# Performance work log

Measured on AMD Instinct MI355X. Metric: run time of the kernel, lower is better.

Reference implementation:

```python
import jax, jax.numpy as jnp
import numpy as np

N = 50000          # num nodes
E = 600000         # num edges
F_IN = 128         # num_features
H = 128            # graph_hidden_dim
R = 2              # num_relations
L = 3              # n_layers_conv
BN_EPS = 1e-5
BN_BETA = 1e-4     # BatchNorm bias init per module code


def setup_inputs() -> dict:
    key = jax.random.key(0)
    ks = jax.random.split(key, 9)
    s_in = 1.0 / np.sqrt(F_IN)
    s_h = 1.0 / np.sqrt(H)
    return {
        "x": jax.random.normal(ks[0], (N, F_IN), jnp.float32),
        "edge_index": jax.random.randint(ks[1], (2, E), 0, N, jnp.int32),
        "edge_type": jax.random.randint(ks[2], (E,), 0, R, jnp.int32),
        "W0_rel": jax.random.normal(ks[3], (R, F_IN, H), jnp.float32) * s_in,
        "W0_root": jax.random.normal(ks[4], (F_IN, H), jnp.float32) * s_in,
        "b0": jnp.zeros((H,), jnp.float32),
        "Ws_rel": jax.random.normal(ks[5], (L, R, H, H), jnp.float32) * s_h,
        "Ws_root": jax.random.normal(ks[6], (L, H, H), jnp.float32) * s_h,
        "bs": jnp.zeros((L, H), jnp.float32),
    }


def batchnorm(x):
    # training-mode BatchNorm1d over nodes; weight=1, bias=1e-4 (per init)
    mu = jnp.mean(x, axis=0)
    var = jnp.mean((x - mu) ** 2, axis=0)  # biased var, as torch uses for norm
    return (x - mu) * jax.lax.rsqrt(var + BN_EPS) + BN_BETA


def rgcn_conv(x, src, dst, edge_type, W_rel, W_root, b):
    # PyG RGCNConv, aggr='mean': per-relation mean of x[src] at dst,
    # then per-relation linear, plus root transform and bias.
    seg = dst * R + edge_type  # combined (node, relation) segment id
    msgs = x[src]                                   # [E, d] gather
    sums = jax.ops.segment_sum(msgs, seg, num_segments=N * R)
    cnts = jax.ops.segment_sum(jnp.ones((src.shape[0],), x.dtype), seg,
                               num_segments=N * R)
    mean = sums.reshape(N, R, -1) / jnp.maximum(cnts, 1.0).reshape(N, R, 1)
    out = jnp.einsum('nrd,rdh->nh', mean, W_rel) + x @ W_root + b
    return out


def reference(x, edge_index, edge_type, W0_rel, W0_root, b0, Ws_rel, Ws_root, bs):
    src, dst = edge_index[0], edge_index[1]
    h = batchnorm(x)
    h = jax.nn.relu(rgcn_conv(h, src, dst, edge_type, W0_rel, W0_root, b0))
    for i in range(L):
        h_ = batchnorm(h)
        h_ = jax.nn.relu(rgcn_conv(h_, src, dst, edge_type,
                                   Ws_rel[i], Ws_root[i], bs[i]))
        h = h + h_  # conv_residual=True
    return h  # gconv_dropout == 0
```

## Files before the change

kernel.cpp:

```cpp
#include <hip/hip_runtime.h>
#include <hip/hip_bf16.h>

#define N_NODES 50000
#define N_EDGES 600000
#define F 128
#define R 2
#define NLAYER 4
#define NSEG (N_NODES * R)
#define SEGP (NSEG / 8)
#define NSCB 98
#define NB 384
#define STATS_STRIDE 2048
#define AGGB 6250
#define BN_EPS 1e-5f
#define BETA 1e-4f

typedef __hip_bfloat16 bf16;
typedef __attribute__((ext_vector_type(8))) short short8;
typedef __attribute__((ext_vector_type(4))) short short4x;
typedef __attribute__((ext_vector_type(4))) float floatx4;

__device__ __forceinline__ float b2f(short s) {
    union { unsigned u; float f; } c;
    c.u = ((unsigned)(unsigned short)s) << 16;
    return c.f;
}

__global__ void k_wt(const float* __restrict__ W0_rel, const float* __restrict__ W0_root,
                     const float* __restrict__ Ws_rel, const float* __restrict__ Ws_root,
                     bf16* __restrict__ Bt) {
    int idx = blockIdx.x * 256 + threadIdx.x;
    if (idx >= NLAYER * NB * F) return;
    int l = idx / (NB * F);
    int rem = idx % (NB * F);
    int j = rem / F, d = rem % F;
    float v;
    if (j < 256) {
        int r = j >> 7, c = j & 127;
        v = (l == 0) ? W0_rel[(r * F + d) * F + c]
                     : Ws_rel[((size_t)((l - 1) * R + r) * F + d) * F + c];
    } else {
        int c = j - 256;
        v = (l == 0) ? W0_root[d * F + c]
                     : Ws_root[((size_t)(l - 1) * F + d) * F + c];
    }
    Bt[idx] = __float2bfloat16(v);
}

__global__ void k_seg(const int* __restrict__ dst, const int* __restrict__ et,
                      int* __restrict__ seg) {
    int e = blockIdx.x * 256 + threadIdx.x;
    if (e < N_EDGES) seg[e] = dst[e] * R + et[e];
}

__global__ void k_count(const int* __restrict__ seg, int* __restrict__ cnt) {
    int g = blockIdx.x & 7;
    int lo = g * SEGP, hi = lo + SEGP;
    for (int e = (blockIdx.x >> 3) * 256 + threadIdx.x; e < N_EDGES; e += 65536) {
        int s = seg[e];
        if (s >= lo && s < hi) atomicAdd(&cnt[s], 1);
    }
}

__global__ void k_scan1(const int* __restrict__ cnt, int* __restrict__ off,
                        int* __restrict__ bsum) {
    int t = threadIdx.x;
    int g = blockIdx.x * 1024 + t;
    int v = (g < NSEG) ? cnt[g] : 0;
    int lane = t & 63;
    int wv = t >> 6;
    int x = v;
    for (int d = 1; d < 64; d <<= 1) {
        int y = __shfl_up(x, d, 64);
        if (lane >= d) x += y;
    }
    __shared__ int wtot[16];
    if (lane == 63) wtot[wv] = x;
    __syncthreads();
    if (t < 16) {
        int s = wtot[t];
        for (int d = 1; d < 16; d <<= 1) {
            int y = __shfl_up(s, d, 64);
            if (t >= d) s += y;
        }
        wtot[t] = s;
    }
    __syncthreads();
    int wpre = (wv == 0) ? 0 : wtot[wv - 1];
    int incl = x + wpre;
    if (g < NSEG) off[g] = incl - v;
    if (t == 1023) bsum[blockIdx.x] = incl;
}

__global__ void k_scan3(int* __restrict__ off, const int* __restrict__ bsum) {
    __shared__ int pre;
    if (threadIdx.x == 0) {
        int p = 0;
        for (int b = 0; b < blockIdx.x; b++) p += bsum[b];
        pre = p;
    }
    __syncthreads();
    int g = blockIdx.x * 1024 + threadIdx.x;
    if (g < NSEG) off[g] += pre;
}

__global__ void k_fill(const int* __restrict__ src, const int* __restrict__ seg,
                       const int* __restrict__ off,
                       int* __restrict__ fill, int* __restrict__ esrc) {
    int g = blockIdx.x & 7;
    int lo = g * SEGP, hi = lo + SEGP;
    for (int e = (blockIdx.x >> 3) * 256 + threadIdx.x; e < N_EDGES; e += 65536) {
        int s = seg[e];
        if (s >= lo && s < hi) {
            int idx = off[s] + atomicAdd(&fill[s], 1);
            esrc[idx] = src[e];
        }
    }
}

__global__ void k_bnstats(const float* __restrict__ h, float* __restrict__ gs) {
    int c = threadIdx.x & 127;
    int rl = threadIdx.x >> 7;
    float s = 0.f, q = 0.f;
    for (int r = blockIdx.x * 2 + rl; r < N_NODES; r += gridDim.x * 2) {
        float v = h[(size_t)r * F + c];
        s += v; q += v * v;
    }
    __shared__ float ls[256], lq[256];
    ls[threadIdx.x] = s; lq[threadIdx.x] = q;
    __syncthreads();
    if (rl == 0) {
        atomicAdd(&gs[c], ls[c] + ls[c + 128]);
        atomicAdd(&gs[128 + c], lq[c] + lq[c + 128]);
    }
}

__launch_bounds__(512)
__global__ void k_gemm(const void* __restrict__ hin, int in_bf16,
                       const float* __restrict__ gs,
                       const bf16* __restrict__ Bt, const float* __restrict__ bias,
                       bf16* __restrict__ y, bf16* __restrict__ z) {
    __shared__ bf16 As[64 * 136];
    __shared__ bf16 Bs[128 * 136];
    int t = threadIdx.x;
    int m0 = blockIdx.x * 64;
    int c4 = (t & 31) * 4;
    float mu[4], rs[4];
    for (int c = 0; c < 4; c++) {
        float ssum = 0.f, qsum = 0.f;
        #pragma unroll
        for (int k = 0; k < 8; k++) {
            ssum += gs[k * 256 + c4 + c];
            qsum += gs[k * 256 + 128 + c4 + c];
        }
        float mm = ssum * (1.0f / N_NODES);
        float qq = qsum * (1.0f / N_NODES);
        mu[c] = mm;
        rs[c] = rsqrtf(qq - mm * mm + BN_EPS);
    }
    short8 cur[4], nxt[4];
    #pragma unroll
    for (int rr = 0; rr < 4; rr++) {
        int idx = rr * 512 + t;
        int row = idx >> 4;
        int kc = idx & 15;
        cur[rr] = *(const short8*)(Bt + row * F + kc * 8);
    }
    int r0 = t >> 5;
    for (int it = 0; it < 4; it++) {
        int row = r0 + it * 16;
        int m = m0 + row;
        float f0 = 0.f, f1 = 0.f, f2 = 0.f, f3 = 0.f;
        if (m < N_NODES) {
            if (in_bf16) {
                short4x v = *(const short4x*)((const bf16*)hin + (size_t)m * F + c4);
                f0 = b2f(v.x); f1 = b2f(v.y); f2 = b2f(v.z); f3 = b2f(v.w);
            } else {
                float4 v = *(const float4*)((const float*)hin + (size_t)m * F + c4);
                f0 = v.x; f1 = v.y; f2 = v.z; f3 = v.w;
            }
        }
        bf16 o[4];
        o[0] = __float2bfloat16((f0 - mu[0]) * rs[0] + BETA);
        o[1] = __float2bfloat16((f1 - mu[1]) * rs[1] + BETA);
        o[2] = __float2bfloat16((f2 - mu[2]) * rs[2] + BETA);
        o[3] = __float2bfloat16((f3 - mu[3]) * rs[3] + BETA);
        *(double*)(As + row * 136 + c4) = *(const double*)o;
    }
    __syncthreads();
    int w = t >> 6;
    int lane = t & 63;
    int msub = w & 3;
    int nh = w >> 2;
    int lm = lane & 15;
    int lq = lane >> 4;
    short8 a[4];
    for (int ki = 0; ki < 4; ki++)
        a[ki] = *(const short8*)(As + (msub * 16 + lm) * 136 + ki * 32 + lq * 8);
    int m = m0 + msub * 16 + lm;
    #pragma unroll
    for (int ci = 0; ci < 3; ci++) {
        #pragma unroll
        for (int rr = 0; rr < 4; rr++) {
            int idx = rr * 512 + t;
            int row = idx >> 4;
            int kc = idx & 15;
            *(short8*)(Bs + row * 136 + kc * 8) = cur[rr];
        }
        if (ci < 2) {
            const bf16* bsrc = Bt + (size_t)(ci + 1) * 128 * F;
            #pragma unroll
            for (int rr = 0; rr < 4; rr++) {
                int idx = rr * 512 + t;
                int row = idx >> 4;
                int kc = idx & 15;
                nxt[rr] = *(const short8*)(bsrc + row * F + kc * 8);
            }
        }
        __syncthreads();
        for (int tt = 0; tt < 4; tt++) {
            int nt = nh * 4 + tt;
            short8 b[4];
            for (int ki = 0; ki < 4; ki++)
                b[ki] = *(const short8*)(Bs + (nt * 16 + lm) * 136 + ki * 32 + lq * 8);
            floatx4 acc = {0.f, 0.f, 0.f, 0.f};
            for (int ki = 0; ki < 4; ki++)
                acc = __builtin_amdgcn_mfma_f32_16x16x32_bf16(b[ki], a[ki], acc, 0, 0, 0);
            int n0 = ci * 128 + nt * 16 + lq * 4;
            if (m < N_NODES) {
                if (ci < 2) {
                    union { bf16 o[4]; double d; } u;
                    u.o[0] = __float2bfloat16(acc[0]);
                    u.o[1] = __float2bfloat16(acc[1]);
                    u.o[2] = __float2bfloat16(acc[2]);
                    u.o[3] = __float2bfloat16(acc[3]);
                    *(double*)(y + (size_t)m * 256 + n0) = u.d;
                } else {
                    float4 bv = *(const float4*)(bias + (n0 - 256));
                    union { bf16 o[4]; double d; } u;
                    u.o[0] = __float2bfloat16(acc[0] + bv.x);
                    u.o[1] = __float2bfloat16(acc[1] + bv.y);
                    u.o[2] = __float2bfloat16(acc[2] + bv.z);
                    u.o[3] = __float2bfloat16(acc[3] + bv.w);
                    *(double*)(z + (size_t)m * F + (n0 - 256)) = u.d;
                }
            }
        }
        if (ci < 2) {
            __syncthreads();
            #pragma unroll
            for (int rr = 0; rr < 4; rr++) cur[rr] = nxt[rr];
        }
    }
}

__launch_bounds__(512)
__global__ void k_aggregate(const bf16* __restrict__ y, const bf16* __restrict__ z,
                            const int* __restrict__ cnt, const int* __restrict__ off,
                            const int* __restrict__ esrc,
                            const bf16* __restrict__ hres, bf16* __restrict__ hb_out,
                            float* __restrict__ out_f32,
                            float* __restrict__ gs_next, int layer) {
    int wid = (blockIdx.x * 512 + threadIdx.x) >> 6;
    int lane = threadIdx.x & 63;
    int n = wid;
    int half = lane >> 5;
    int hl = lane & 31;
    int c4 = hl * 4;
    int2 cc = *(const int2*)(cnt + n * R);
    int o0 = off[n * R];
    int myc = half ? cc.y : cc.x;
    int myo = half ? (o0 + cc.x) : o0;
    float myinv = (myc > 0) ? 1.0f / (float)myc : 0.f;
    const bf16* yb = y + half * 128 + c4;
    float s0 = 0.f, s1 = 0.f, s2 = 0.f, s3 = 0.f;
    for (int i = 0; i < myc; i += 8) {
        int sn[8];
        #pragma unroll
        for (int k = 0; k < 8; k++) {
            int valid = (i + k < myc);
            sn[k] = esrc[valid ? (myo + i + k) : myo];
        }
        short4x p[8];
        #pragma unroll
        for (int k = 0; k < 8; k++)
            p[k] = *(const short4x*)(yb + (size_t)sn[k] * 256);
        #pragma unroll
        for (int k = 0; k < 8; k++) {
            float wk = (i + k < myc) ? myinv : 0.f;
            s0 = fmaf(b2f(p[k].x), wk, s0);
            s1 = fmaf(b2f(p[k].y), wk, s1);
            s2 = fmaf(b2f(p[k].z), wk, s2);
            s3 = fmaf(b2f(p[k].w), wk, s3);
        }
    }
    float t0 = __shfl_xor(s0, 32, 64);
    float t1 = __shfl_xor(s1, 32, 64);
    float t2 = __shfl_xor(s2, 32, 64);
    float t3 = __shfl_xor(s3, 32, 64);
    __shared__ float ls[8][128], lq[8][128];
    int wv = threadIdx.x >> 6;
    if (half == 0) {
        short4x zb = *(const short4x*)(z + (size_t)n * F + c4);
        float4 hp = {0.f, 0.f, 0.f, 0.f};
        if (layer > 0) {
            short4x hv = *(const short4x*)(hres + (size_t)n * F + c4);
            hp.x = b2f(hv.x); hp.y = b2f(hv.y); hp.z = b2f(hv.z); hp.w = b2f(hv.w);
        }
        float4 o4;
        o4.x = fmaxf(b2f(zb.x) + s0 + t0, 0.f) + hp.x;
        o4.y = fmaxf(b2f(zb.y) + s1 + t1, 0.f) + hp.y;
        o4.z = fmaxf(b2f(zb.z) + s2 + t2, 0.f) + hp.z;
        o4.w = fmaxf(b2f(zb.w) + s3 + t3, 0.f) + hp.w;
        if (out_f32) {
            *(float4*)(out_f32 + (size_t)n * F + c4) = o4;
        } else {
            bf16 ob[4];
            ob[0] = __float2bfloat16(o4.x);
            ob[1] = __float2bfloat16(o4.y);
            ob[2] = __float2bfloat16(o4.z);
            ob[3] = __float2bfloat16(o4.w);
            *(double*)(hb_out + (size_t)n * F + c4) = *(const double*)ob;
            if (gs_next) {
                float r0v = b2f(*(const short*)&ob[0]);
                float r1v = b2f(*(const short*)&ob[1]);
                float r2v = b2f(*(const short*)&ob[2]);
                float r3v = b2f(*(const short*)&ob[3]);
                ls[wv][c4 + 0] = r0v; ls[wv][c4 + 1] = r1v;
                ls[wv][c4 + 2] = r2v; ls[wv][c4 + 3] = r3v;
                lq[wv][c4 + 0] = r0v * r0v; lq[wv][c4 + 1] = r1v * r1v;
                lq[wv][c4 + 2] = r2v * r2v; lq[wv][c4 + 3] = r3v * r3v;
            }
        }
    }
    if (gs_next) {
        __syncthreads();
        int t = threadIdx.x;
        float* gsc = gs_next + (blockIdx.x & 7) * 256;
        if (t < 128) {
            float S = ((ls[0][t] + ls[1][t]) + (ls[2][t] + ls[3][t]))
                    + ((ls[4][t] + ls[5][t]) + (ls[6][t] + ls[7][t]));
            atomicAdd(&gsc[t], S);
        } else if (t < 256) {
            int c = t - 128;
            float Q = ((lq[0][c] + lq[1][c]) + (lq[2][c] + lq[3][c]))
                    + ((lq[4][c] + lq[5][c]) + (lq[6][c] + lq[7][c]));
            atomicAdd(&gsc[128 + c], Q);
        }
    }
}

extern "C" void kernel_launch(void* const* d_in, const int* in_sizes, int n_in,
                              void* d_out, int out_size, void* d_ws, size_t ws_size,
                              hipStream_t stream) {
    const float* x       = (const float*)d_in[0];
    const int*   eidx    = (const int*)d_in[1];
    const int*   etype   = (const int*)d_in[2];
    const float* W0_rel  = (const float*)d_in[3];
    const float* W0_root = (const float*)d_in[4];
    const float* b0      = (const float*)d_in[5];
    const float* Ws_rel  = (const float*)d_in[6];
    const float* Ws_root = (const float*)d_in[7];
    const float* bs      = (const float*)d_in[8];
    const int* src = eidx;
    const int* dst = eidx + N_EDGES;

    char* w = (char*)d_ws;
    bf16*  hb  = (bf16*)w;  w += (size_t)N_NODES * F * 2;
    bf16*  z   = (bf16*)w;  w += (size_t)N_NODES * F * 2;
    bf16*  y   = (bf16*)w;  w += (size_t)N_NODES * 256 * 2;
    bf16*  Bt  = (bf16*)w;  w += (size_t)NLAYER * NB * F * 2;
    int* cnt   = (int*)w;   w += (size_t)NSEG * 4;
    int* fill  = (int*)w;   w += (size_t)NSEG * 4;
    float* stats = (float*)w; w += (size_t)NLAYER * STATS_STRIDE * 4;
    int* off   = (int*)w;   w += (size_t)NSEG * 4;
    int* esrc  = (int*)w;   w += (size_t)N_EDGES * 4;
    int* segb  = (int*)w;   w += (size_t)N_EDGES * 4;
    int* bsum  = (int*)w;   w += 128 * 4;

    hipMemsetAsync(cnt, 0, (size_t)NSEG * 4 * 2 + (size_t)NLAYER * STATS_STRIDE * 4, stream);
    k_wt<<<(NLAYER * NB * F + 255) / 256, 256, 0, stream>>>(W0_rel, W0_root, Ws_rel, Ws_root, Bt);
    k_seg<<<(N_EDGES + 255) / 256, 256, 0, stream>>>(dst, etype, segb);
    k_count<<<2048, 256, 0, stream>>>(segb, cnt);
    k_scan1<<<NSCB, 1024, 0, stream>>>(cnt, off, bsum);
    k_scan3<<<NSCB, 1024, 0, stream>>>(off, bsum);
    k_fill<<<2048, 256, 0, stream>>>(src, segb, off, fill, esrc);
    k_bnstats<<<512, 256, 0, stream>>>(x, stats);

    for (int l = 0; l < NLAYER; l++) {
        const float* gsl = stats + (size_t)l * STATS_STRIDE;
        const float* bias = (l == 0) ? b0 : (bs + (size_t)(l - 1) * F);
        const void* hin = (l == 0) ? (const void*)x : (const void*)hb;
        k_gemm<<<(N_NODES + 63) / 64, 512, 0, stream>>>(
            hin, (l > 0) ? 1 : 0, gsl, Bt + (size_t)l * NB * F, bias, y, z);
        k_aggregate<<<AGGB, 512, 0, stream>>>(
            y, z, cnt, off, esrc, hb, hb,
            (l == 3) ? (float*)d_out : nullptr,
            (l < 3) ? (float*)(stats + (size_t)(l + 1) * STATS_STRIDE) : nullptr, l);
    }
}
```

Measured before the change: 417.7 us.

## Pre-partition edges into 8 segment buckets before count and fill

Replaces the segment-id kernel with a partition pass that computes each edge's segment and scatters (segment, src) pairs into 8 bucket arrays by segment range. The count and fill kernels then walk only their own bucket instead of scanning all edges 8 times with a range filter. This removes redundant full-edge reads in the CSR build, at the cost of an extra scatter pass and a fixed per-bucket capacity (PCAP) that assumes a balanced distribution.

```diff
diff --git a/kernel.cpp b/kernel.cpp
--- a/kernel.cpp
+++ b/kernel.cpp
@@ -12,6 +12,8 @@
 #define NB 384
 #define STATS_STRIDE 2048
 #define AGGB 6250
+#define PCAP 76800
+#define PARTB 512
 #define BN_EPS 1e-5f
 #define BETA 1e-4f
 
@@ -47,19 +49,43 @@
     Bt[idx] = __float2bfloat16(v);
 }
 
-__global__ void k_seg(const int* __restrict__ dst, const int* __restrict__ et,
-                      int* __restrict__ seg) {
-    int e = blockIdx.x * 256 + threadIdx.x;
-    if (e < N_EDGES) seg[e] = dst[e] * R + et[e];
-}
-
-__global__ void k_count(const int* __restrict__ seg, int* __restrict__ cnt) {
+__global__ void k_part(const int* __restrict__ dst, const int* __restrict__ et,
+                       const int* __restrict__ src,
+                       int* __restrict__ eseg, int* __restrict__ esrcb,
+                       int* __restrict__ bcnt) {
+    __shared__ int hist[8], base[8], cur[8];
+    int t = threadIdx.x;
+    if (t < 8) hist[t] = 0;
+    __syncthreads();
+    int per = (N_EDGES + PARTB - 1) / PARTB;
+    int e0 = blockIdx.x * per;
+    int e1 = e0 + per; if (e1 > N_EDGES) e1 = N_EDGES;
+    for (int e = e0 + t; e < e1; e += 256) {
+        int s = dst[e] * R + et[e];
+        atomicAdd(&hist[s / SEGP], 1);
+    }
+    __syncthreads();
+    if (t < 8) {
+        base[t] = atomicAdd(&bcnt[t], hist[t]);
+        cur[t] = 0;
+    }
+    __syncthreads();
+    for (int e = e0 + t; e < e1; e += 256) {
+        int s = dst[e] * R + et[e];
+        int g = s / SEGP;
+        int idx = g * PCAP + base[g] + atomicAdd(&cur[g], 1);
+        eseg[idx] = s;
+        esrcb[idx] = src[e];
+    }
+}
+
+__global__ void k_count(const int* __restrict__ eseg, const int* __restrict__ bcnt,
+                        int* __restrict__ cnt) {
     int g = blockIdx.x & 7;
-    int lo = g * SEGP, hi = lo + SEGP;
-    for (int e = (blockIdx.x >> 3) * 256 + threadIdx.x; e < N_EDGES; e += 65536) {
-        int s = seg[e];
-        if (s >= lo && s < hi) atomicAdd(&cnt[s], 1);
-    }
+    int n = bcnt[g];
+    const int* p = eseg + (size_t)g * PCAP;
+    for (int i = (blockIdx.x >> 3) * 256 + threadIdx.x; i < n; i += 65536)
+        atomicAdd(&cnt[p[i]], 1);
 }
 
 __global__ void k_scan1(const int* __restrict__ cnt, int* __restrict__ off,
@@ -104,17 +130,17 @@
     if (g < NSEG) off[g] += pre;
 }
 
-__global__ void k_fill(const int* __restrict__ src, const int* __restrict__ seg,
-                       const int* __restrict__ off,
+__global__ void k_fill(const int* __restrict__ eseg, const int* __restrict__ esrcb,
+                       const int* __restrict__ bcnt, const int* __restrict__ off,
                        int* __restrict__ fill, int* __restrict__ esrc) {
     int g = blockIdx.x & 7;
-    int lo = g * SEGP, hi = lo + SEGP;
-    for (int e = (blockIdx.x >> 3) * 256 + threadIdx.x; e < N_EDGES; e += 65536) {
-        int s = seg[e];
-        if (s >= lo && s < hi) {
-            int idx = off[s] + atomicAdd(&fill[s], 1);
-            esrc[idx] = src[e];
-        }
+    int n = bcnt[g];
+    const int* ps = eseg + (size_t)g * PCAP;
+    const int* pr = esrcb + (size_t)g * PCAP;
+    for (int i = (blockIdx.x >> 3) * 256 + threadIdx.x; i < n; i += 65536) {
+        int s = ps[i];
+        int idx = off[s] + atomicAdd(&fill[s], 1);
+        esrc[idx] = pr[i];
     }
 }
 
@@ -373,18 +399,21 @@
     int* cnt   = (int*)w;   w += (size_t)NSEG * 4;
     int* fill  = (int*)w;   w += (size_t)NSEG * 4;
     float* stats = (float*)w; w += (size_t)NLAYER * STATS_STRIDE * 4;
+    int* bcnt  = (int*)w;   w += 8 * 4;
     int* off   = (int*)w;   w += (size_t)NSEG * 4;
     int* esrc  = (int*)w;   w += (size_t)N_EDGES * 4;
-    int* segb  = (int*)w;   w += (size_t)N_EDGES * 4;
+    int* eseg  = (int*)w;   w += (size_t)PCAP * 8 * 4;
+    int* esrcb = (int*)w;   w += (size_t)PCAP * 8 * 4;
     int* bsum  = (int*)w;   w += 128 * 4;
 
-    hipMemsetAsync(cnt, 0, (size_t)NSEG * 4 * 2 + (size_t)NLAYER * STATS_STRIDE * 4, stream);
+    hipMemsetAsync(cnt, 0,
+        (size_t)NSEG * 4 * 2 + (size_t)NLAYER * STATS_STRIDE * 4 + 8 * 4, stream);
     k_wt<<<(NLAYER * NB * F + 255) / 256, 256, 0, stream>>>(W0_rel, W0_root, Ws_rel, Ws_root, Bt);
-    k_seg<<<(N_EDGES + 255) / 256, 256, 0, stream>>>(dst, etype, segb);
-    k_count<<<2048, 256, 0, stream>>>(segb, cnt);
+    k_part<<<PARTB, 256, 0, stream>>>(dst, etype, src, eseg, esrcb, bcnt);
+    k_count<<<2048, 256, 0, stream>>>(eseg, bcnt, cnt);
     k_scan1<<<NSCB, 1024, 0, stream>>>(cnt, off, bsum);
     k_scan3<<<NSCB, 1024, 0, stream>>>(off, bsum);
-    k_fill<<<2048, 256, 0, stream>>>(src, segb, off, fill, esrc);
+    k_fill<<<2048, 256, 0, stream>>>(eseg, esrcb, bcnt, off, fill, esrc);
     k_bnstats<<<512, 256, 0, stream>>>(x, stats);
 
     for (int l = 0; l < NLAYER; l++) {
```

Result: slower. 429.7 us (+2.9%).
